# Performance work log

Hardware: AMD Instinct MI355X
Metric: run time of the kernel (lower is better)

Reference implementation:

```python
import jax, jax.numpy as jnp
from jax import lax
import numpy as np

DN = ('NCDHW', 'OIDHW', 'NCDHW')
EPS = 1e-3  # BatchNorm1d eps=0.001
GRID = (41, 512, 512)  # spatial_shape [40,512,512] + [1,0,0]


def _block(x, mask, w, gamma, beta, rmean, rvar, stride, padding):
    # Regular (non-submanifold) sparse conv computes the same values as a dense
    # conv on the zero-filled grid; active OUTPUT sites are exactly those reached
    # by any active input site through the kernel window. BN+ReLU act only on
    # active sites (inactive sites stay exactly 0), hence the mask multiply.
    y = lax.conv_general_dilated(x, w, stride, padding, dimension_numbers=DN)
    k1 = jnp.ones((1, 1) + w.shape[2:], x.dtype)
    m = lax.conv_general_dilated(mask, k1, stride, padding, dimension_numbers=DN)
    m = (m > 0).astype(x.dtype)
    inv = gamma / jnp.sqrt(rvar + EPS)
    scale = inv.reshape(1, -1, 1, 1, 1)
    shift = (beta - rmean * inv).reshape(1, -1, 1, 1, 1)
    return jax.nn.relu(y * scale + shift) * m, m


def setup_inputs() -> dict:
    key = jax.random.key(0)
    NV, B = 120000, 2
    kf, kb, kz, ky, kx, kp = jax.random.split(key, 6)
    voxel_features = jax.random.normal(kf, (NV, 3), jnp.float32)
    coors = jnp.stack([
        jax.random.randint(kb, (NV,), 0, B, jnp.int32),
        jax.random.randint(kz, (NV,), 0, 40, jnp.int32),
        jax.random.randint(ky, (NV,), 0, 512, jnp.int32),
        jax.random.randint(kx, (NV,), 0, 512, jnp.int32)], axis=1)
    inp = {"voxel_features": voxel_features, "coors": coors, "batch_size": B}
    chans = [(3, 16, (3, 3, 3)), (16, 32, (3, 3, 3)), (32, 64, (3, 3, 3)), (64, 64, (3, 1, 1))]
    for i, (ci, co, k) in enumerate(chans, 1):
        kw, kg, kbb, km, kv = jax.random.split(jax.random.fold_in(kp, i), 5)
        fan = ci * k[0] * k[1] * k[2]
        inp[f"w{i}"] = jax.random.normal(kw, (co, ci) + k, jnp.float32) / np.sqrt(fan).astype(np.float32)
        inp[f"g{i}"] = jax.random.uniform(kg, (co,), jnp.float32, 0.5, 1.5)
        inp[f"bb{i}"] = jax.random.normal(kbb, (co,), jnp.float32) * 0.1
        inp[f"rm{i}"] = jax.random.normal(km, (co,), jnp.float32) * 0.1
        inp[f"rv{i}"] = jax.random.uniform(kv, (co,), jnp.float32, 0.5, 1.5)
    return inp


def reference(voxel_features, coors, batch_size,
              w1, g1, bb1, rm1, rv1,
              w2, g2, bb2, rm2, rv2,
              w3, g3, bb3, rm3, rv3,
              w4, g4, bb4, rm4, rv4):
    D, H, W = GRID
    C = voxel_features.shape[1]
    b, z, y, x = coors[:, 0], coors[:, 1], coors[:, 2], coors[:, 3]
    dense = jnp.zeros((batch_size, C, D, H, W), voxel_features.dtype)
    dense = dense.at[b, :, z, y, x].add(voxel_features)  # scatter voxels to grid
    mask = jnp.zeros((batch_size, 1, D, H, W), voxel_features.dtype).at[b, 0, z, y, x].set(1.0)
    h, m = _block(dense, mask, w1, g1, bb1, rm1, rv1, (2, 2, 2), [(1, 1), (1, 1), (1, 1)])
    h, m = _block(h, m, w2, g2, bb2, rm2, rv2, (2, 2, 2), [(1, 1), (1, 1), (1, 1)])
    h, m = _block(h, m, w3, g3, bb3, rm3, rv3, (2, 2, 2), [(0, 0), (1, 1), (1, 1)])
    h, m = _block(h, m, w4, g4, bb4, rm4, rv4, (2, 1, 1), [(0, 0), (0, 0), (0, 0)])
    N, Co, Dd, Hh, Ww = h.shape  # [B, 64, 2, 64, 64]
    return h.reshape(N, Co * Dd, Hh, Ww)
```

## Files before the change

kernel.cpp:

```cpp
#include <hip/hip_runtime.h>

#define EPS 1e-3f


typedef _Float16 f16x8 __attribute__((ext_vector_type(8)));
typedef _Float16 h2 __attribute__((ext_vector_type(2)));
typedef float f32x4 __attribute__((ext_vector_type(4)));
typedef float f32x16 __attribute__((ext_vector_type(16)));

#define SLACK_BYTE 2752512
#define SLACK_Y1   90832912

__global__ __launch_bounds__(256) void repack_prezero(
    const float* __restrict__ g1, const float* __restrict__ b1,
    const float* __restrict__ rm1, const float* __restrict__ rv1,
    const float* __restrict__ w2, const float* __restrict__ g2, const float* __restrict__ b2,
    const float* __restrict__ rm2, const float* __restrict__ rv2,
    const float* __restrict__ w3, const float* __restrict__ g3, const float* __restrict__ b3,
    const float* __restrict__ rm3, const float* __restrict__ rv3,
    const float* __restrict__ w4, const float* __restrict__ g4, const float* __restrict__ b4,
    const float* __restrict__ rm4, const float* __restrict__ rv4,
    _Float16* __restrict__ wB2, _Float16* __restrict__ wB3,
    _Float16* __restrict__ wB4, float* __restrict__ shb,
    const int* __restrict__ coors, int NV, unsigned short* __restrict__ y1,
    unsigned char* __restrict__ m1, float* __restrict__ m3)
{
    if (blockIdx.x >= 1034) {
        const int i = (blockIdx.x - 1034) * 256 + threadIdx.x;
        if (i < NV) {
            const int b = coors[4 * i + 0];
            const int z = coors[4 * i + 1];
            const int y = coors[4 * i + 2];
            const int x = coors[4 * i + 3];
            int ozv[2], nz = 0, oyv[2], ny = 0, oxv[2], nx = 0;
#pragma unroll
            for (int k = 0; k < 3; ++k) {
                int t = z + 1 - k;
                if (t >= 0 && !(t & 1)) { int o = t >> 1; if (o < 21) ozv[nz++] = o; }
            }
#pragma unroll
            for (int k = 0; k < 3; ++k) {
                int t = y + 1 - k;
                if (t >= 0 && !(t & 1)) { int o = t >> 1; if (o < 256) oyv[ny++] = o; }
            }
#pragma unroll
            for (int k = 0; k < 3; ++k) {
                int t = x + 1 - k;
                if (t >= 0 && !(t & 1)) { int o = t >> 1; if (o < 256) oxv[nx++] = o; }
            }
            const uint4 zz = {0u, 0u, 0u, 0u};
            for (int a = 0; a < nz; ++a)
                for (int bb = 0; bb < ny; ++bb)
                    for (int c = 0; c < nx; ++c) {
                        const int sp = ozv[a] * 65536 + oyv[bb] * 256 + oxv[c];
                        uint4* p = (uint4*)(y1 + (size_t)(b * 1376256 + sp) * 16);
                        p[0] = zz;
                        p[1] = zz;
                    }
        }
        asm volatile("s_waitcnt vmcnt(0)" ::: "memory");
        return;
    }
    if (blockIdx.x >= 321) {
        const int idx16 = (blockIdx.x - 321) * 256 + threadIdx.x;
        const uint4 zz = {0u, 0u, 0u, 0u};
        if (idx16 < 172034) {
            ((uint4*)m1)[idx16] = zz;
        } else if (idx16 < 182274) {
            ((uint4*)m3)[idx16 - 172034] = zz;
        }
        return;
    }

    const int i = blockIdx.x * 256 + threadIdx.x;
    if (i < 13824) {
        const int j = i & 7, lane = (i >> 3) & 63, tap = i >> 9;
        const int oc = lane & 31;
        const int cin = (lane >> 5) * 8 + j;
        const float inv = g2[oc] * rsqrtf(rv2[oc] + EPS);
        wB2[i] = (_Float16)(w2[(oc * 16 + cin) * 27 + tap] * inv);
    } else if (i >= 14336 && i < 69632) {
        const int j2 = i - 14336;
        const int j = j2 & 7, lane = (j2 >> 3) & 63, t = (j2 >> 9) & 3, tap = j2 >> 11;
        const int q = lane >> 4, n = lane & 15;
        const int oc = t * 16 + n;
        const int cin = q * 8 + j;
        const float inv = g3[oc] * rsqrtf(rv3[oc] + EPS);
        wB3[j2] = (_Float16)(w3[(oc * 32 + cin) * 27 + tap] * inv);
    } else if (i >= 69632 && i < 81920) {
        const int j2 = i - 69632;
        const int j = j2 & 7, lane = (j2 >> 3) & 63, t = (j2 >> 9) & 3, c = j2 >> 11;
        const int q = lane >> 4, n = lane & 15;
        const int oc = t * 16 + n;
        const int k = c * 32 + q * 8 + j;
        const int dz = k >> 6, cin = k & 63;
        const float inv = g4[oc] * rsqrtf(rv4[oc] + EPS);
        wB4[j2] = (_Float16)(w4[(oc * 64 + cin) * 3 + dz] * inv);
    } else if (i >= 81920 && i < 82128) {
        const int j = i - 81920;
        if (j < 32) {
            const float inv = g2[j] * rsqrtf(rv2[j] + EPS);
            shb[j] = b2[j] - rm2[j] * inv;
        } else if (j < 96) {
            const int o = j - 32;
            const float inv = g3[o] * rsqrtf(rv3[o] + EPS);
            shb[j] = b3[o] - rm3[o] * inv;
        } else if (j < 160) {
            const int o = j - 96;
            const float inv = g4[o] * rsqrtf(rv4[o] + EPS);
            shb[j] = b4[o] - rm4[o] * inv;
        } else if (j < 176) {
            const int o = j - 160;
            shb[j] = g1[o] * rsqrtf(rv1[o] + EPS);
        } else if (j < 192) {
            const int o = j - 176;
            const float inv = g1[o] * rsqrtf(rv1[o] + EPS);
            shb[j] = b1[o] - rm1[o] * inv;
        } else if (j < 200) {
            const int o = j - 192;
            const int c0 = 2 * o, c1 = 2 * o + 1;
            const float i0 = g1[c0] * rsqrtf(rv1[c0] + EPS);
            const float i1 = g1[c1] * rsqrtf(rv1[c1] + EPS);
            const float s0 = b1[c0] - rm1[c0] * i0;
            const float s1 = b1[c1] - rm1[c1] * i1;
            const unsigned lo = (unsigned)__builtin_bit_cast(unsigned short, (_Float16)s0);
            const unsigned hi = (unsigned)__builtin_bit_cast(unsigned short, (_Float16)s1);
            shb[j] = __uint_as_float(lo | (hi << 16));
        }
    }
}

__global__ __launch_bounds__(256) void scatter_l1(
    const float* __restrict__ vf, const int* __restrict__ coors, int NV,
    const float* __restrict__ w1, const float* __restrict__ shb,
    unsigned short* __restrict__ y1, unsigned char* __restrict__ m1)
{
    __shared__ float ws[16 * 3 * 27];
    for (int e = threadIdx.x; e < 16 * 3 * 27; e += 256)
        ws[e] = w1[e] * shb[160 + e / 81];
    __syncthreads();

    const int gid = blockIdx.x * 256 + threadIdx.x;
    const int i = gid >> 3;
    const int oc2 = gid & 7;
    if (i < NV) {
        const int oc = oc2 * 2;

        const int b = coors[4 * i + 0];
        const int z = coors[4 * i + 1];
        const int y = coors[4 * i + 2];
        const int x = coors[4 * i + 3];
        const float f0 = vf[3 * i + 0];
        const float f1 = vf[3 * i + 1];
        const float f2 = vf[3 * i + 2];

        int ozv[2], kzv[2], nz = 0;
        int oyv[2], kyv[2], ny = 0;
        int oxv[2], kxv[2], nx = 0;
#pragma unroll
        for (int k = 0; k < 3; ++k) {
            int t = z + 1 - k;
            if (t >= 0 && !(t & 1)) { int o = t >> 1; if (o < 21) { ozv[nz] = o; kzv[nz] = k; ++nz; } }
        }
#pragma unroll
        for (int k = 0; k < 3; ++k) {
            int t = y + 1 - k;
            if (t >= 0 && !(t & 1)) { int o = t >> 1; if (o < 256) { oyv[ny] = o; kyv[ny] = k; ++ny; } }
        }
#pragma unroll
        for (int k = 0; k < 3; ++k) {
            int t = x + 1 - k;
            if (t >= 0 && !(t & 1)) { int o = t >> 1; if (o < 256) { oxv[nx] = o; kxv[nx] = k; ++nx; } }
        }

        for (int a = 0; a < nz; ++a)
            for (int bb = 0; bb < ny; ++bb)
                for (int c = 0; c < nx; ++c) {
                    const int oz = ozv[a], oy = oyv[bb], ox = oxv[c];
                    const int tap = (kzv[a] * 3 + kyv[bb]) * 3 + kxv[c];
                    const int sp = oz * 65536 + oy * 256 + ox;
                    if (oc2 == 0) m1[b * 1376256 + sp] = 1;
                    const float s0 = ws[oc * 81 + tap] * f0 + ws[oc * 81 + 27 + tap] * f1 +
                                     ws[oc * 81 + 54 + tap] * f2;
                    const float s1 = ws[(oc + 1) * 81 + tap] * f0 +
                                     ws[(oc + 1) * 81 + 27 + tap] * f1 +
                                     ws[(oc + 1) * 81 + 54 + tap] * f2;
                    const unsigned pk = __builtin_bit_cast(
                        unsigned, __builtin_amdgcn_cvt_pkrtz(s0, s1));
                    unsigned* addr = (unsigned*)(y1 + (size_t)(b * 1376256 + sp) * 16 +
                                                 oc2 * 2);
                    asm volatile("global_atomic_pk_add_f16 %0, %1, off"
                                 : : "v"(addr), "v"(pk) : "memory");
                }
    }
    asm volatile("s_waitcnt vmcnt(0)" ::: "memory");
}

__global__ __launch_bounds__(256) void masks_pass(
    const unsigned char* __restrict__ m1, float* __restrict__ m2,
    float* __restrict__ m3)
{
    const int idx = blockIdx.x * 256 + threadIdx.x;
    const int b = idx / 180224;
    const int r = idx - b * 180224;
    const int oz = r >> 14, r2 = r & 16383, oy = r2 >> 7, ox = r2 & 127;
    const int iz0 = 2 * oz - 1, iyb = 2 * oy - 1, ixb = 2 * ox - 1;
    unsigned msum = 0;
#pragma unroll
    for (int kz = 0; kz < 3; ++kz) {
        const int iz = iz0 + kz;
#pragma unroll
        for (int ky = 0; ky < 3; ++ky) {
            const int iy = iyb + ky;
#pragma unroll
            for (int kx = 0; kx < 3; ++kx) {
                const int ix = ixb + kx;
                if ((unsigned)iz < 21u && (unsigned)iy < 256u &&
                    (unsigned)ix < 256u)
                    msum |= m1[b * 1376256 + iz * 65536 + iy * 256 + ix];
            }
        }
    }
    m2[idx] = msum ? 1.f : 0.f;

    if (msum) {
        int ozv[2], nz = 0, oyv[2], ny = 0, oxv[2], nx = 0;
#pragma unroll
        for (int k = 0; k < 3; ++k) {
            int t = oz - k;
            if (t >= 0 && !(t & 1)) { int o = t >> 1; if (o < 5) ozv[nz++] = o; }
        }
#pragma unroll
        for (int k = 0; k < 3; ++k) {
            int t = oy + 1 - k;
            if (t >= 0 && !(t & 1)) { int o = t >> 1; if (o < 64) oyv[ny++] = o; }
        }
#pragma unroll
        for (int k = 0; k < 3; ++k) {
            int t = ox + 1 - k;
            if (t >= 0 && !(t & 1)) { int o = t >> 1; if (o < 64) oxv[nx++] = o; }
        }
        for (int a = 0; a < nz; ++a)
            for (int bb = 0; bb < ny; ++bb)
                for (int c = 0; c < nx; ++c)
                    m3[b * 20480 + ozv[a] * 4096 + oyv[bb] * 64 + oxv[c]] = 1.0f;
    }
}

__global__ __launch_bounds__(256) __attribute__((amdgpu_waves_per_eu(4, 8)))
void conv_l2(
    const unsigned char* __restrict__ y1c,
    const unsigned char* __restrict__ m1,
    const uint4* __restrict__ wB2,
    const float* __restrict__ m2, const float* __restrict__ shb,
    _Float16* __restrict__ h2h)
{
    __shared__ uint4 lds4[3 * 520];
    unsigned char* lds = (unsigned char*)lds4;

    const int tid = threadIdx.x;
    const int lane = tid & 63;
    const int w = tid >> 6;
    const int m = lane & 31, h = lane >> 5;

    const int sbid = (blockIdx.x & 7) * 352 + (blockIdx.x >> 3);
    const int oy = sbid / 22;
    const int plane = sbid - oy * 22;
    const int b = plane / 11, oz = plane - b * 11;

    const int ox0 = w * 32;
    const int iz0 = 2 * oz - 1, iyb = 2 * oy - 1;
    const int bbase = b * 1376256;
    const int qoff = h * 16;

    const int shalf = tid & 1;

    unsigned shp[4];
    {
        const uint4 sv = *(const uint4*)((const unsigned char*)(shb + 192) + shalf * 16);
        shp[0] = sv.x; shp[1] = sv.y; shp[2] = sv.z; shp[3] = sv.w;
    }

    int rdo[3];
#pragma unroll
    for (int kx = 0; kx < 3; ++kx) {
        const unsigned L = (unsigned)((2 * (ox0 + m) + kx) * 32 + qoff);
        rdo[kx] = (int)(L ^ (((L >> 7) & 7u) << 4));
    }

    int st_lws[7], st_y1b[7], st_m1o[7];
    bool st_ok[7], st_vrow[7];
#pragma unroll
    for (int it = 0; it < 7; ++it) {
        const int l = it * 256 + tid;
        st_ok[it] = l < 1560;
        const int row = l / 520;
        const int u = l - row * 520;
        const int lx = u >> 1;
        const int ix = lx - 1;
        const int iy = iyb + row;
        st_vrow[it] = (unsigned)iy < 256u && (unsigned)ix < 256u;
        const int cell0 = bbase + iz0 * 65536 + iy * 256 + ix;
        st_y1b[it] = cell0 * 32 + shalf * 16;
        st_m1o[it] = cell0;
        const unsigned Ll = (unsigned)(lx * 32 + shalf * 16);
        st_lws[it] = row * 8320 + (int)(Ll ^ (((Ll >> 7) & 7u) << 4));
    }

    const h2 z2 = {(_Float16)0.f, (_Float16)0.f};

    f32x16 acc;
#pragma unroll
    for (int r = 0; r < 16; ++r) acc[r] = 0.f;

    for (int kz = 0; kz < 3; ++kz) {
        const bool izok = (unsigned)(iz0 + kz) < 21u;
        const int kzb = kz * 2097152;
        const int kzc = kz * 65536;

        __syncthreads();
        uint4 sd[7];
        unsigned char sm[7];
#pragma unroll
        for (int it = 0; it < 7; ++it) {
            if (st_ok[it]) {
                const bool v = izok && st_vrow[it];
                sd[it] = *(const uint4*)(y1c +
                          (v ? (st_y1b[it] + kzb) : (int)SLACK_Y1));
                sm[it] = m1[v ? (st_m1o[it] + kzc) : SLACK_BYTE];
            }
        }
#pragma unroll
        for (int it = 0; it < 7; ++it) {
            if (st_ok[it]) {
                const bool act = sm[it] != 0;
                unsigned od[4];
                const unsigned dvs[4] = {sd[it].x, sd[it].y, sd[it].z, sd[it].w};
#pragma unroll
                for (int jj = 0; jj < 4; ++jj) {
                    const h2 v = __builtin_bit_cast(h2, dvs[jj]);
                    const h2 s = __builtin_bit_cast(h2, shp[jj]);
                    const h2 r = __builtin_elementwise_max(v + s, z2);
                    od[jj] = act ? __builtin_bit_cast(unsigned, r) : 0u;
                }
                const uint4 uc = {od[0], od[1], od[2], od[3]};
                *(uint4*)(lds + st_lws[it]) = uc;
            }
        }
        __syncthreads();

#pragma unroll
        for (int ky = 0; ky < 3; ++ky) {
#pragma unroll
            for (int kx = 0; kx < 3; ++kx) {
                const int tap = kz * 9 + ky * 3 + kx;
                const uint4 ua = *(const uint4*)(lds + ky * 8320 + rdo[kx]);
                const f16x8 af = __builtin_bit_cast(f16x8, ua);
                const f16x8 bf = __builtin_bit_cast(f16x8, wB2[tap * 64 + lane]);
                acc = __builtin_amdgcn_mfma_f32_32x32x16_f16(af, bf, acc, 0, 0, 0);
            }
        }
    }

    const int oc = lane & 31;
#pragma unroll
    for (int r = 0; r < 16; ++r) {
        const int row = (r & 3) + 8 * (r >> 2) + 4 * h;
        const int px = ox0 + row;
        const int spo = oz * 16384 + oy * 128 + px;
        const float mv = m2[b * 180224 + spo];
        const size_t cbase = (size_t)(b * 180224 + spo) * 32;
        h2h[cbase + oc] = (_Float16)(fmaxf(acc[r] + shb[oc], 0.f) * mv);
    }
}

__global__ __launch_bounds__(256) __attribute__((amdgpu_waves_per_eu(4, 8)))
void conv_l3(
    const unsigned char* __restrict__ h2h,
    const uint4* __restrict__ wB3,
    const float* __restrict__ m3, const float* __restrict__ shb,
    _Float16* __restrict__ h3h)
{
    const int tid = threadIdx.x;
    const int gw = blockIdx.x * 4 + (tid >> 6);
    const int lane = tid & 63;
    const int m = lane & 15, q = lane >> 4;

    const int plane = gw >> 8;
    const int rem = gw & 255;
    const int oy = rem >> 2;
    const int ox0 = (rem & 3) * 16;
    const int b = plane / 5, oz = plane % 5;
    const int iz0 = 2 * oz, iyb = 2 * oy - 1;
    const int ixm = 2 * (ox0 + m) - 1;
    const int bbase = b * 180224;
    const int qoff = q * 16;

    f32x4 acc[4];
#pragma unroll
    for (int t = 0; t < 4; ++t) acc[t] = (f32x4){0.f, 0.f, 0.f, 0.f};

    uint4 buf[9];
    bool  val[9];
#pragma unroll
    for (int t = 0; t < 9; ++t) {
        const int ky = (t / 3) % 3, kx = t % 3;
        const int iz = iz0 + t / 9, iy = iyb + ky, ix = ixm + kx;
        const bool v = (unsigned)iy < 128u && (unsigned)ix < 128u;
        const int cell = bbase + iz * 16384 + iy * 128 + ix;
        buf[t] = *(const uint4*)(h2h + (v ? (cell * 64 + qoff) : 0));
        val[t] = v;
    }

#pragma unroll
    for (int tap = 0; tap < 27; ++tap) {
        const int s = tap % 9;
        uint4 ua = buf[s];
        if (!val[s]) { ua.x = 0; ua.y = 0; ua.z = 0; ua.w = 0; }
        if (tap + 9 < 27) {
            const int t2 = tap + 9;
            const int kz = t2 / 9, ky = (t2 / 3) % 3, kx = t2 % 3;
            const int iz = iz0 + kz, iy = iyb + ky, ix = ixm + kx;
            const bool v = (unsigned)iy < 128u && (unsigned)ix < 128u;
            const int cell = bbase + iz * 16384 + iy * 128 + ix;
            buf[s] = *(const uint4*)(h2h + (v ? (cell * 64 + qoff) : 0));
            val[s] = v;
        }
        const f16x8 af = __builtin_bit_cast(f16x8, ua);
#pragma unroll
        for (int t = 0; t < 4; ++t) {
            const f16x8 bf = __builtin_bit_cast(f16x8, wB3[(tap * 4 + t) * 64 + lane]);
            acc[t] = __builtin_amdgcn_mfma_f32_16x16x32_f16(af, bf, acc[t], 0, 0, 0);
        }
    }

    const int n = lane & 15;
#pragma unroll
    for (int r = 0; r < 4; ++r) {
        const int px = ox0 + q * 4 + r;
        const int spo = oz * 4096 + oy * 64 + px;
        const float mv = m3[b * 20480 + spo];
        const size_t cb = (size_t)(b * 20480 + spo) * 64;
#pragma unroll
        for (int t = 0; t < 4; ++t) {
            const int oc = t * 16 + n;
            h3h[cb + oc] = (_Float16)(fmaxf(acc[t][r] + shb[32 + oc], 0.f) * mv);
        }
    }
}

__global__ __launch_bounds__(256) __attribute__((amdgpu_waves_per_eu(4, 8)))
void conv_l4(
    const unsigned char* __restrict__ h3h,
    const uint4* __restrict__ wB4,
    const float* __restrict__ m3, const float* __restrict__ shb,
    float* __restrict__ out)
{
    const int tid = threadIdx.x;
    const int gw = blockIdx.x * 4 + (tid >> 6);
    const int lane = tid & 63;
    const int m = lane & 15, q = lane >> 4;

    const int b = gw >> 9, od = (gw >> 8) & 1;
    const int oy = (gw >> 2) & 63, ox0 = (gw & 3) * 16;
    const int cellbase = (b * 5 + 2 * od) * 4096 + oy * 64 + ox0 + m;

    f32x4 acc[4];
#pragma unroll
    for (int t = 0; t < 4; ++t) acc[t] = (f32x4){0.f, 0.f, 0.f, 0.f};

#pragma unroll
    for (int c = 0; c < 6; ++c) {
        const int dz = c >> 1;
        const size_t addr = (size_t)(cellbase + dz * 4096) * 128 +
                            (c & 1) * 64 + q * 16;
        const uint4 ua = *(const uint4*)(h3h + addr);
        const f16x8 af = __builtin_bit_cast(f16x8, ua);
#pragma unroll
        for (int t = 0; t < 4; ++t) {
            const f16x8 bf = __builtin_bit_cast(f16x8, wB4[(c * 4 + t) * 64 + lane]);
            acc[t] = __builtin_amdgcn_mfma_f32_16x16x32_f16(af, bf, acc[t], 0, 0, 0);
        }
    }

    const int n = lane & 15;
#pragma unroll
    for (int r = 0; r < 4; ++r) {
        const int px = ox0 + q * 4 + r;
        const int spo = oy * 64 + px;
        const float msum = m3[(b * 5 + 2 * od + 0) * 4096 + spo] +
                           m3[(b * 5 + 2 * od + 1) * 4096 + spo] +
                           m3[(b * 5 + 2 * od + 2) * 4096 + spo];
        const float mv = msum > 0.f ? 1.f : 0.f;
#pragma unroll
        for (int t = 0; t < 4; ++t) {
            const int oc = t * 16 + n;
            out[((b * 64 + oc) * 2 + od) * 4096 + spo] =
                fmaxf(acc[t][r] + shb[96 + oc], 0.f) * mv;
        }
    }
}

extern "C" void kernel_launch(void* const* d_in, const int* in_sizes, int n_in,
                              void* d_out, int out_size, void* d_ws, size_t ws_size,
                              hipStream_t stream)
{
    const float* vf    = (const float*)d_in[0];
    const int*   coors = (const int*)d_in[1];
    const float* w1 = (const float*)d_in[3];
    const float* g1 = (const float*)d_in[4];
    const float* b1 = (const float*)d_in[5];
    const float* rm1 = (const float*)d_in[6];
    const float* rv1 = (const float*)d_in[7];
    const float* w2 = (const float*)d_in[8];
    const float* g2 = (const float*)d_in[9];
    const float* b2 = (const float*)d_in[10];
    const float* rm2 = (const float*)d_in[11];
    const float* rv2 = (const float*)d_in[12];
    const float* w3 = (const float*)d_in[13];
    const float* g3 = (const float*)d_in[14];
    const float* b3 = (const float*)d_in[15];
    const float* rm3 = (const float*)d_in[16];
    const float* rv3 = (const float*)d_in[17];
    const float* w4 = (const float*)d_in[18];
    const float* g4 = (const float*)d_in[19];
    const float* b4 = (const float*)d_in[20];
    const float* rm4 = (const float*)d_in[21];
    const float* rv4 = (const float*)d_in[22];

    const int NV = in_sizes[0] / 3;

    float* ws = (float*)d_ws;
    float* y1  = ws;
    float* m1f = y1 + 22020096;
    float* h2h = m1f + 2752512;
    float* m2  = h2h + 5767168;
    float* h3h = m2 + 360448;
    float* m3  = h3h + 1310720;
    float* wB2 = m3 + 40960;
    float* wB3 = wB2 + 7168;
    float* wB4 = wB3 + 27648;
    float* shb = wB4 + 6144;

    unsigned char* m1 = (unsigned char*)m1f;

    const int pzBlocks = (NV + 255) / 256;
    repack_prezero<<<1034 + pzBlocks, 256, 0, stream>>>(
        g1, b1, rm1, rv1,
        w2, g2, b2, rm2, rv2, w3, g3, b3, rm3, rv3,
        w4, g4, b4, rm4, rv4,
        (_Float16*)wB2, (_Float16*)wB3, (_Float16*)wB4, shb,
        coors, NV, (unsigned short*)y1, m1, m3);
    scatter_l1<<<(NV * 8 + 255) / 256, 256, 0, stream>>>(vf, coors, NV, w1, shb,
                                                         (unsigned short*)y1, m1);
    masks_pass<<<1408, 256, 0, stream>>>(m1, m2, m3);
    conv_l2<<<2816, 256, 0, stream>>>((const unsigned char*)d_ws, m1,
                                      (const uint4*)wB2, m2, shb, (_Float16*)h2h);
    conv_l3<<<640, 256, 0, stream>>>((const unsigned char*)h2h, (const uint4*)wB3,
                                     m3, shb, (_Float16*)h3h);
    conv_l4<<<256, 256, 0, stream>>>((const unsigned char*)h3h, (const uint4*)wB4,
                                     m3, shb, (float*)d_out);
}
```

Measured before the change: 226.5 us.

## Double-buffer LDS in conv_l2 to overlap global loads with MFMA

Doubles the LDS staging buffer in conv_l2 and software-pipelines the three kz slices: global loads for the next slice are issued before the MFMA work on the current slice, and the next slice is written into the alternate buffer. This removes one barrier per iteration and is meant to hide global-memory latency behind matrix compute. In exchange it doubles LDS use (about 50KB per block), which may lower occupancy, and keeps more registers live across the MFMA loop.

```diff
diff --git a/kernel.cpp b/kernel.cpp
--- a/kernel.cpp
+++ b/kernel.cpp
@@ -255,7 +255,7 @@
     const float* __restrict__ m2, const float* __restrict__ shb,
     _Float16* __restrict__ h2h)
 {
-    __shared__ uint4 lds4[3 * 520];
+    __shared__ uint4 lds4[2 * 3 * 520];
     unsigned char* lds = (unsigned char*)lds4;
 
     const int tid = threadIdx.x;
@@ -313,54 +313,80 @@
 #pragma unroll
     for (int r = 0; r < 16; ++r) acc[r] = 0.f;
 
-    for (int kz = 0; kz < 3; ++kz) {
-        const bool izok = (unsigned)(iz0 + kz) < 21u;
-        const int kzb = kz * 2097152;
-        const int kzc = kz * 65536;
-
-        __syncthreads();
-        uint4 sd[7];
-        unsigned char sm[7];
-#pragma unroll
-        for (int it = 0; it < 7; ++it) {
-            if (st_ok[it]) {
-                const bool v = izok && st_vrow[it];
-                sd[it] = *(const uint4*)(y1c +
-                          (v ? (st_y1b[it] + kzb) : (int)SLACK_Y1));
-                sm[it] = m1[v ? (st_m1o[it] + kzc) : SLACK_BYTE];
-            }
-        }
-#pragma unroll
-        for (int it = 0; it < 7; ++it) {
-            if (st_ok[it]) {
-                const bool act = sm[it] != 0;
-                unsigned od[4];
-                const unsigned dvs[4] = {sd[it].x, sd[it].y, sd[it].z, sd[it].w};
-#pragma unroll
-                for (int jj = 0; jj < 4; ++jj) {
-                    const h2 v = __builtin_bit_cast(h2, dvs[jj]);
-                    const h2 s = __builtin_bit_cast(h2, shp[jj]);
-                    const h2 r = __builtin_elementwise_max(v + s, z2);
-                    od[jj] = act ? __builtin_bit_cast(unsigned, r) : 0u;
-                }
-                const uint4 uc = {od[0], od[1], od[2], od[3]};
-                *(uint4*)(lds + st_lws[it]) = uc;
-            }
-        }
-        __syncthreads();
-
-#pragma unroll
-        for (int ky = 0; ky < 3; ++ky) {
-#pragma unroll
-            for (int kx = 0; kx < 3; ++kx) {
-                const int tap = kz * 9 + ky * 3 + kx;
-                const uint4 ua = *(const uint4*)(lds + ky * 8320 + rdo[kx]);
-                const f16x8 af = __builtin_bit_cast(f16x8, ua);
-                const f16x8 bf = __builtin_bit_cast(f16x8, wB2[tap * 64 + lane]);
-                acc = __builtin_amdgcn_mfma_f32_32x32x16_f16(af, bf, acc, 0, 0, 0);
-            }
-        }
-    }
+    uint4 sd[7];
+    unsigned char sm[7];
+
+#define L2_ISSUE(KZ)                                                          \
+    {                                                                         \
+        const bool izok_ = (unsigned)(iz0 + (KZ)) < 21u;                      \
+        _Pragma("unroll")                                                     \
+        for (int it = 0; it < 7; ++it) {                                      \
+            if (st_ok[it]) {                                                  \
+                const bool v_ = izok_ && st_vrow[it];                         \
+                sd[it] = *(const uint4*)(y1c +                                \
+                    (v_ ? (st_y1b[it] + (KZ) * 2097152) : (int)SLACK_Y1));    \
+                sm[it] = m1[v_ ? (st_m1o[it] + (KZ) * 65536) : SLACK_BYTE];   \
+            }                                                                 \
+        }                                                                     \
+    }
+
+#define L2_WRITE(PB)                                                          \
+    {                                                                         \
+        _Pragma("unroll")                                                     \
+        for (int it = 0; it < 7; ++it) {                                      \
+            if (st_ok[it]) {                                                  \
+                const bool act_ = sm[it] != 0;                                \
+                unsigned od_[4];                                              \
+                const unsigned dv0_ = sd[it].x, dv1_ = sd[it].y,              \
+                               dv2_ = sd[it].z, dv3_ = sd[it].w;              \
+                const unsigned dvs_[4] = {dv0_, dv1_, dv2_, dv3_};            \
+                _Pragma("unroll")                                             \
+                for (int jj = 0; jj < 4; ++jj) {                              \
+                    const h2 vv_ = __builtin_bit_cast(h2, dvs_[jj]);          \
+                    const h2 ss_ = __builtin_bit_cast(h2, shp[jj]);           \
+                    const h2 rr_ = __builtin_elementwise_max(vv_ + ss_, z2);  \
+                    od_[jj] = act_ ? __builtin_bit_cast(unsigned, rr_) : 0u;  \
+                }                                                             \
+                const uint4 uc_ = {od_[0], od_[1], od_[2], od_[3]};           \
+                *(uint4*)(lds + (PB) * 24960 + st_lws[it]) = uc_;             \
+            }                                                                 \
+        }                                                                     \
+    }
+
+#define L2_CONSUME(KZ, PB)                                                    \
+    {                                                                         \
+        _Pragma("unroll")                                                     \
+        for (int ky = 0; ky < 3; ++ky) {                                      \
+            _Pragma("unroll")                                                 \
+            for (int kx = 0; kx < 3; ++kx) {                                  \
+                const int tap_ = (KZ) * 9 + ky * 3 + kx;                      \
+                const uint4 ua_ = *(const uint4*)(lds + (PB) * 24960 +        \
+                                                  ky * 8320 + rdo[kx]);       \
+                const f16x8 af_ = __builtin_bit_cast(f16x8, ua_);             \
+                const f16x8 bf_ = __builtin_bit_cast(f16x8,                   \
+                                                     wB2[tap_ * 64 + lane]);  \
+                acc = __builtin_amdgcn_mfma_f32_32x32x16_f16(af_, bf_, acc,   \
+                                                             0, 0, 0);        \
+            }                                                                 \
+        }                                                                     \
+    }
+
+    L2_ISSUE(0)
+    L2_WRITE(0)
+    __syncthreads();
+    L2_ISSUE(1)
+    L2_CONSUME(0, 0)
+    L2_WRITE(1)
+    __syncthreads();
+    L2_ISSUE(2)
+    L2_CONSUME(1, 1)
+    L2_WRITE(0)
+    __syncthreads();
+    L2_CONSUME(2, 0)
+
+#undef L2_ISSUE
+#undef L2_WRITE
+#undef L2_CONSUME
 
     const int oc = lane & 31;
 #pragma unroll
```

After: 228.3 us. No clear change (+0.8%).

## Prefetch all three kz slabs up front and double-buffer LDS in conv_l2

Applied to the files above, without the earlier changes.

conv_l2 now issues the global loads for all three kz input slices at the start, stages two slices into a doubled LDS buffer, and keeps the third in registers. The third is written to LDS only after the first two slices' MFMAs have run. This cuts the number of load-then-barrier round trips from three to fewer and lets memory latency overlap with compute. In exchange it uses much more register and LDS space, and the occupancy hint drops to waves_per_eu(2), which lowers occupancy.

```diff
diff --git a/kernel.cpp b/kernel.cpp
--- a/kernel.cpp
+++ b/kernel.cpp
@@ -247,7 +247,7 @@
     }
 }
 
-__global__ __launch_bounds__(256) __attribute__((amdgpu_waves_per_eu(4, 8)))
+__global__ __launch_bounds__(256) __attribute__((amdgpu_waves_per_eu(2)))
 void conv_l2(
     const unsigned char* __restrict__ y1c,
     const unsigned char* __restrict__ m1,
@@ -255,7 +255,7 @@
     const float* __restrict__ m2, const float* __restrict__ shb,
     _Float16* __restrict__ h2h)
 {
-    __shared__ uint4 lds4[3 * 520];
+    __shared__ uint4 lds4[2 * 3 * 520];
     unsigned char* lds = (unsigned char*)lds4;
 
     const int tid = threadIdx.x;
@@ -309,56 +309,129 @@
 
     const h2 z2 = {(_Float16)0.f, (_Float16)0.f};
 
+    uint4 sd0[7], sd1[7], sd2[7];
+    unsigned sm0[7], sm1[7], sm2[7];
+    const bool iz0ok = (unsigned)(iz0 + 0) < 21u;
+    const bool iz1ok = (unsigned)(iz0 + 1) < 21u;
+    const bool iz2ok = (unsigned)(iz0 + 2) < 21u;
+#pragma unroll
+    for (int it = 0; it < 7; ++it) {
+        if (st_ok[it]) {
+            const bool v = iz0ok && st_vrow[it];
+            sd0[it] = *(const uint4*)(y1c + (v ? st_y1b[it] : (int)SLACK_Y1));
+            sm0[it] = m1[v ? st_m1o[it] : SLACK_BYTE];
+        }
+    }
+#pragma unroll
+    for (int it = 0; it < 7; ++it) {
+        if (st_ok[it]) {
+            const bool v = iz1ok && st_vrow[it];
+            sd1[it] = *(const uint4*)(y1c + (v ? (st_y1b[it] + 2097152) : (int)SLACK_Y1));
+            sm1[it] = m1[v ? (st_m1o[it] + 65536) : SLACK_BYTE];
+        }
+    }
+#pragma unroll
+    for (int it = 0; it < 7; ++it) {
+        if (st_ok[it]) {
+            const bool v = iz2ok && st_vrow[it];
+            sd2[it] = *(const uint4*)(y1c + (v ? (st_y1b[it] + 4194304) : (int)SLACK_Y1));
+            sm2[it] = m1[v ? (st_m1o[it] + 131072) : SLACK_BYTE];
+        }
+    }
+
+#pragma unroll
+    for (int it = 0; it < 7; ++it) {
+        if (st_ok[it]) {
+            const bool act = sm0[it] != 0;
+            unsigned od[4];
+            const unsigned dvs[4] = {sd0[it].x, sd0[it].y, sd0[it].z, sd0[it].w};
+#pragma unroll
+            for (int jj = 0; jj < 4; ++jj) {
+                const h2 vv = __builtin_bit_cast(h2, dvs[jj]);
+                const h2 ss = __builtin_bit_cast(h2, shp[jj]);
+                const h2 rr = __builtin_elementwise_max(vv + ss, z2);
+                od[jj] = act ? __builtin_bit_cast(unsigned, rr) : 0u;
+            }
+            const uint4 uc = {od[0], od[1], od[2], od[3]};
+            *(uint4*)(lds + st_lws[it]) = uc;
+        }
+    }
+#pragma unroll
+    for (int it = 0; it < 7; ++it) {
+        if (st_ok[it]) {
+            const bool act = sm1[it] != 0;
+            unsigned od[4];
+            const unsigned dvs[4] = {sd1[it].x, sd1[it].y, sd1[it].z, sd1[it].w};
+#pragma unroll
+            for (int jj = 0; jj < 4; ++jj) {
+                const h2 vv = __builtin_bit_cast(h2, dvs[jj]);
+                const h2 ss = __builtin_bit_cast(h2, shp[jj]);
+                const h2 rr = __builtin_elementwise_max(vv + ss, z2);
+                od[jj] = act ? __builtin_bit_cast(unsigned, rr) : 0u;
+            }
+            const uint4 uc = {od[0], od[1], od[2], od[3]};
+            *(uint4*)(lds + 24960 + st_lws[it]) = uc;
+        }
+    }
+
+#pragma unroll
+    for (int it = 0; it < 7; ++it) {
+        asm volatile("" : "+v"(sd2[it].x), "+v"(sd2[it].y),
+                          "+v"(sd2[it].z), "+v"(sd2[it].w), "+v"(sm2[it]));
+    }
+
+    __syncthreads();
+
     f32x16 acc;
 #pragma unroll
     for (int r = 0; r < 16; ++r) acc[r] = 0.f;
 
-    for (int kz = 0; kz < 3; ++kz) {
-        const bool izok = (unsigned)(iz0 + kz) < 21u;
-        const int kzb = kz * 2097152;
-        const int kzc = kz * 65536;
-
-        __syncthreads();
-        uint4 sd[7];
-        unsigned char sm[7];
-#pragma unroll
-        for (int it = 0; it < 7; ++it) {
-            if (st_ok[it]) {
-                const bool v = izok && st_vrow[it];
-                sd[it] = *(const uint4*)(y1c +
-                          (v ? (st_y1b[it] + kzb) : (int)SLACK_Y1));
-                sm[it] = m1[v ? (st_m1o[it] + kzc) : SLACK_BYTE];
-            }
-        }
-#pragma unroll
-        for (int it = 0; it < 7; ++it) {
-            if (st_ok[it]) {
-                const bool act = sm[it] != 0;
-                unsigned od[4];
-                const unsigned dvs[4] = {sd[it].x, sd[it].y, sd[it].z, sd[it].w};
-#pragma unroll
-                for (int jj = 0; jj < 4; ++jj) {
-                    const h2 v = __builtin_bit_cast(h2, dvs[jj]);
-                    const h2 s = __builtin_bit_cast(h2, shp[jj]);
-                    const h2 r = __builtin_elementwise_max(v + s, z2);
-                    od[jj] = act ? __builtin_bit_cast(unsigned, r) : 0u;
-                }
-                const uint4 uc = {od[0], od[1], od[2], od[3]};
-                *(uint4*)(lds + st_lws[it]) = uc;
-            }
-        }
-        __syncthreads();
-
+#pragma unroll
+    for (int kz = 0; kz < 2; ++kz) {
 #pragma unroll
         for (int ky = 0; ky < 3; ++ky) {
 #pragma unroll
             for (int kx = 0; kx < 3; ++kx) {
                 const int tap = kz * 9 + ky * 3 + kx;
-                const uint4 ua = *(const uint4*)(lds + ky * 8320 + rdo[kx]);
+                const uint4 ua = *(const uint4*)(lds + kz * 24960 + ky * 8320 + rdo[kx]);
                 const f16x8 af = __builtin_bit_cast(f16x8, ua);
                 const f16x8 bf = __builtin_bit_cast(f16x8, wB2[tap * 64 + lane]);
                 acc = __builtin_amdgcn_mfma_f32_32x32x16_f16(af, bf, acc, 0, 0, 0);
             }
+        }
+    }
+
+    __syncthreads();
+
+#pragma unroll
+    for (int it = 0; it < 7; ++it) {
+        if (st_ok[it]) {
+            const bool act = sm2[it] != 0;
+            unsigned od[4];
+            const unsigned dvs[4] = {sd2[it].x, sd2[it].y, sd2[it].z, sd2[it].w};
+#pragma unroll
+            for (int jj = 0; jj < 4; ++jj) {
+                const h2 vv = __builtin_bit_cast(h2, dvs[jj]);
+                const h2 ss = __builtin_bit_cast(h2, shp[jj]);
+                const h2 rr = __builtin_elementwise_max(vv + ss, z2);
+                od[jj] = act ? __builtin_bit_cast(unsigned, rr) : 0u;
+            }
+            const uint4 uc = {od[0], od[1], od[2], od[3]};
+            *(uint4*)(lds + st_lws[it]) = uc;
+        }
+    }
+
+    __syncthreads();
+
+#pragma unroll
+    for (int ky = 0; ky < 3; ++ky) {
+#pragma unroll
+        for (int kx = 0; kx < 3; ++kx) {
+            const int tap = 18 + ky * 3 + kx;
+            const uint4 ua = *(const uint4*)(lds + ky * 8320 + rdo[kx]);
+            const f16x8 af = __builtin_bit_cast(f16x8, ua);
+            const f16x8 bf = __builtin_bit_cast(f16x8, wB2[tap * 64 + lane]);
+            acc = __builtin_amdgcn_mfma_f32_32x32x16_f16(af, bf, acc, 0, 0, 0);
         }
     }
 
```

Result: no change. 226.2 us (-0.1%).
